# Performance work log

Hardware: AMD Instinct MI355X
Metric: run time of the kernel (lower is better)

The kernel has to match this reference:

```python
import jax, jax.numpy as jnp
import numpy as np

N, E, F, H, EF, ED, L, NL, NH, OD = 2048, 65536, 128, 512, 16, 64, 5, 4, 8, 64
MAX_DEG = 64


def _ln(x, s, b):
    m = x.mean(-1, keepdims=True)
    v = x.var(-1, keepdims=True)
    return (x - m) * jax.lax.rsqrt(v + 1e-5) * s + b


def setup_inputs() -> dict:
    key = jax.random.key(0)
    ks = jax.random.split(key, 40)
    s = 0.02
    x = jax.random.normal(ks[0], (N, F), jnp.float32)
    edge_index = jax.random.randint(ks[1], (2, E), 0, N, jnp.int32)
    edge_attr = jax.random.normal(ks[2], (E, EF), jnp.float32)
    # variable-length shortest paths, padded with -1
    plen = jax.random.randint(ks[3], (N, N), 0, L + 1, jnp.int32)
    pos = jnp.arange(L, dtype=jnp.int32)
    valid = pos[None, None, :] < plen[:, :, None]
    node_paths = jnp.where(valid, jax.random.randint(ks[4], (N, N, L), 0, N, jnp.int32), -1)
    edge_paths = jnp.where(valid, jax.random.randint(ks[5], (N, N, L), 0, E, jnp.int32), -1)
    p = {
        'x': x, 'edge_index': edge_index, 'edge_attr': edge_attr,
        'node_paths': node_paths, 'edge_paths': edge_paths,
        'W_node': s * jax.random.normal(ks[6], (F, H)), 'b_node': jnp.zeros((H,)),
        'W_edge': s * jax.random.normal(ks[7], (EF, ED)), 'b_edge': jnp.zeros((ED,)),
        'z_in': s * jax.random.normal(ks[8], (MAX_DEG, H)),
        'z_out': s * jax.random.normal(ks[9], (MAX_DEG, H)),
        'b_spatial': s * jax.random.normal(ks[10], (L,)),
        'edge_vector': s * jax.random.normal(ks[11], (L, ED)),
        'ln1_s': jnp.ones((NL, H)), 'ln1_b': jnp.zeros((NL, H)),
        'Wq': s * jax.random.normal(ks[12], (NL, H, H)), 'bq': jnp.zeros((NL, H)),
        'Wk': s * jax.random.normal(ks[13], (NL, H, H)), 'bk': jnp.zeros((NL, H)),
        'Wv': s * jax.random.normal(ks[14], (NL, H, H)), 'bv': jnp.zeros((NL, H)),
        'Wo': s * jax.random.normal(ks[15], (NL, H, H)), 'bo': jnp.zeros((NL, H)),
        'ln2_s': jnp.ones((NL, H)), 'ln2_b': jnp.zeros((NL, H)),
        'W1': s * jax.random.normal(ks[16], (NL, H, H)), 'b1': jnp.zeros((NL, H)),
        'W2': s * jax.random.normal(ks[17], (NL, H, H)), 'b2': jnp.zeros((NL, H)),
        'W_out': s * jax.random.normal(ks[18], (H, OD)), 'b_out': jnp.zeros((OD,)),
    }
    return p


def reference(x, edge_index, edge_attr, node_paths, edge_paths,
              W_node, b_node, W_edge, b_edge, z_in, z_out, b_spatial, edge_vector,
              ln1_s, ln1_b, Wq, bq, Wk, bk, Wv, bv, Wo, bo,
              ln2_s, ln2_b, W1, b1, W2, b2, W_out, b_out):
    n = x.shape[0]
    dk = H // NH
    h = x @ W_node + b_node  # [N,H]
    # centrality encoding: in/out degree -> learned embeddings, clamped
    in_deg = jnp.clip(jnp.zeros((n,), jnp.int32).at[edge_index[1]].add(1), 0, MAX_DEG - 1)
    out_deg = jnp.clip(jnp.zeros((n,), jnp.int32).at[edge_index[0]].add(1), 0, MAX_DEG - 1)
    h = h + z_in[in_deg] + z_out[out_deg]
    # edge encoding: mean over path of <edge_vector[k], edge_emb[path_k]>
    e_emb = edge_attr @ W_edge + b_edge           # [E,ED]
    w = e_emb @ edge_vector.T                     # [E,L] per-position dot products
    valid_e = edge_paths >= 0
    gath = w[jnp.clip(edge_paths, 0), jnp.arange(L)[None, None, :]]  # [N,N,L]
    cnt = valid_e.sum(-1).astype(h.dtype)
    c = jnp.where(cnt > 0, (gath * valid_e).sum(-1) / jnp.maximum(cnt, 1.0), 0.0)  # [N,N]
    # spatial encoding: learned scalar per path length
    plen = (node_paths >= 0).sum(-1)
    b_sp = jnp.where(plen > 0, b_spatial[jnp.clip(plen - 1, 0, L - 1)], 0.0)  # [N,N]
    bias = b_sp + c
    scale = 1.0 / jnp.sqrt(jnp.asarray(dk, h.dtype))
    for l in range(NL):
        y = _ln(h, ln1_s[l], ln1_b[l])
        q = (y @ Wq[l] + bq[l]).reshape(n, NH, dk)
        k = (y @ Wk[l] + bk[l]).reshape(n, NH, dk)
        v = (y @ Wv[l] + bv[l]).reshape(n, NH, dk)
        scores = jnp.einsum('ihd,jhd->hij', q, k) * scale + bias[None]
        attn = jax.nn.softmax(scores, axis=-1)
        o = jnp.einsum('hij,jhd->ihd', attn, v).reshape(n, H)
        h = h + o @ Wo[l] + bo[l]
        y2 = _ln(h, ln2_s[l], ln2_b[l])
        h = h + jax.nn.gelu(y2 @ W1[l] + b1[l]) @ W2[l] + b2[l]
    return h @ W_out + b_out
```

## Files before the change

### kernel.cpp

```cpp
#include <hip/hip_runtime.h>
#include <hip/hip_bf16.h>
#include <math.h>

#define N_NODES 2048
#define NEDGE   65536
#define FDIM    128
#define HDIM    512
#define EFD     16
#define EDD     64
#define LPATH   5
#define NLAYER  4
#define NHEAD   8
#define DK      64
#define ODIM    64
#define MAXDEG  64
#define PHALF   2097152

typedef __bf16 bf16;
typedef bf16 bf16x8 __attribute__((ext_vector_type(8)));
typedef bf16 bf16x4 __attribute__((ext_vector_type(4)));
typedef float f32x4 __attribute__((ext_vector_type(4)));
typedef unsigned short u16;
typedef u16 u16x4 __attribute__((ext_vector_type(4)));


__global__ void k_edge_mat(const float* __restrict__ W_edge, const float* __restrict__ b_edge,
                           const float* __restrict__ ev, float* __restrict__ M, float* __restrict__ c5) {
    int t = threadIdx.x;
    if (t < EFD * LPATH) {
        int i = t / LPATH, j = t % LPATH;
        float acc = 0.f;
        for (int k = 0; k < EDD; ++k) acc += W_edge[i * EDD + k] * ev[j * EDD + k];
        M[t] = acc;
    } else if (t >= 80 && t < 80 + LPATH) {
        int j = t - 80;
        float acc = 0.f;
        for (int k = 0; k < EDD; ++k) acc += b_edge[k] * ev[j * EDD + k];
        c5[j] = acc;
    }
}

__global__ __launch_bounds__(256) void k_edge_w(const float* __restrict__ ea, const float* __restrict__ M,
                                                const float* __restrict__ c5, bf16* __restrict__ wT) {
    __shared__ float sM[80];
    __shared__ float sc[8];
    int t = threadIdx.x;
    if (t < 80) sM[t] = M[t];
    if (t < LPATH) sc[t] = c5[t];
    __syncthreads();
    int e = blockIdx.x * 256 + t;
    const float4* p = (const float4*)(ea + (size_t)e * EFD);
    float4 a0 = p[0], a1 = p[1], a2 = p[2], a3 = p[3];
    float a[16] = {a0.x, a0.y, a0.z, a0.w, a1.x, a1.y, a1.z, a1.w,
                   a2.x, a2.y, a2.z, a2.w, a3.x, a3.y, a3.z, a3.w};
    float out[LPATH];
#pragma unroll
    for (int j = 0; j < LPATH; ++j) out[j] = sc[j];
#pragma unroll
    for (int i = 0; i < 16; ++i)
#pragma unroll
        for (int j = 0; j < LPATH; ++j) out[j] += a[i] * sM[i * LPATH + j];
#pragma unroll
    for (int j = 0; j < LPATH; ++j) wT[(size_t)j * NEDGE + e] = (bf16)out[j];
}

__global__ __launch_bounds__(256) void k_deg(const int* __restrict__ ei, int* __restrict__ din, int* __restrict__ dout) {
    int e = blockIdx.x * 256 + threadIdx.x;
    if (e < NEDGE) {
        atomicAdd(&dout[ei[e]], 1);
        atomicAdd(&din[ei[NEDGE + e]], 1);
    }
}

__global__ __launch_bounds__(256) void k_pack(const int* __restrict__ ep, u16* __restrict__ idxp,
                                              unsigned char* __restrict__ maskp) {
    int tid4 = blockIdx.x * 256 + threadIdx.x;
    const int4* p = (const int4*)(ep + (size_t)tid4 * 20);
    int4 q0 = p[0], q1 = p[1], q2 = p[2], q3 = p[3], q4 = p[4];
    int e[20] = {q0.x, q0.y, q0.z, q0.w, q1.x, q1.y, q1.z, q1.w,
                 q2.x, q2.y, q2.z, q2.w, q3.x, q3.y, q3.z, q3.w,
                 q4.x, q4.y, q4.z, q4.w};
    u16x4 out[LPATH];
    unsigned m[4] = {0, 0, 0, 0};
#pragma unroll
    for (int pp = 0; pp < 4; ++pp) {
#pragma unroll
        for (int l = 0; l < LPATH; ++l) {
            int v = e[pp * 5 + l];
            if (v >= 0) m[pp] |= (1u << l);
            out[l][pp] = (u16)v;
        }
    }
#pragma unroll
    for (int l = 0; l < LPATH; ++l)
        *(u16x4*)(idxp + (size_t)l * PHALF + tid4 * 4) = out[l];
    unsigned packed = m[0] | (m[1] << 8) | (m[2] << 16) | (m[3] << 24);
    *(unsigned*)(maskp + (size_t)tid4 * 4) = packed;
}

__global__ __launch_bounds__(1024) void k_bias2(const u16* __restrict__ idxp, const unsigned char* __restrict__ maskp,
                                                const bf16* __restrict__ wT, const float* __restrict__ bsp,
                                                bf16* __restrict__ bias) {
    __shared__ bf16 wsl[NEDGE];
    int t = threadIdx.x;
    int base = blockIdx.x * 8192;
    unsigned char msk[8];
    float csum[8] = {};
#pragma unroll
    for (int r = 0; r < 8; ++r) msk[r] = maskp[base + r * 1024 + t];
    for (int l = 0; l < LPATH; ++l) {
        __syncthreads();
#pragma unroll
        for (int u = 0; u < 4; ++u) {
            int o = u * 16384 + t * 16;
            *(bf16x8*)&wsl[o]     = *(const bf16x8*)&wT[(size_t)l * NEDGE + o];
            *(bf16x8*)&wsl[o + 8] = *(const bf16x8*)&wT[(size_t)l * NEDGE + o + 8];
        }
        u16 ei[8];
#pragma unroll
        for (int r = 0; r < 8; ++r) ei[r] = idxp[(size_t)l * PHALF + base + r * 1024 + t];
        __syncthreads();
#pragma unroll
        for (int r = 0; r < 8; ++r) {
            float v = (float)wsl[ei[r]];
            csum[r] += ((msk[r] >> l) & 1) ? v : 0.f;
        }
    }
#pragma unroll
    for (int r = 0; r < 8; ++r) {
        int cnt = __popc((int)msk[r]);
        float b = cnt ? bsp[cnt - 1] + csum[r] / (float)cnt : 0.f;
        bias[base + r * 1024 + t] = (bf16)b;
    }
}

__global__ __launch_bounds__(256) void k_ln(const float* __restrict__ h, const float* __restrict__ sc,
                                            const float* __restrict__ bi, bf16* __restrict__ y) {
    int i = blockIdx.x, t = threadIdx.x;
    float v0 = h[(size_t)i * HDIM + t];
    float v1 = h[(size_t)i * HDIM + 256 + t];
    float s = v0 + v1, q = v0 * v0 + v1 * v1;
#pragma unroll
    for (int m = 1; m < 64; m <<= 1) { s += __shfl_xor(s, m); q += __shfl_xor(q, m); }
    __shared__ float ssum[4], sq[4];
    int wv = t >> 6;
    if ((t & 63) == 0) { ssum[wv] = s; sq[wv] = q; }
    __syncthreads();
    float S = ssum[0] + ssum[1] + ssum[2] + ssum[3];
    float Q = sq[0] + sq[1] + sq[2] + sq[3];
    float mean = S * (1.f / HDIM);
    float var = Q * (1.f / HDIM) - mean * mean;
    float r = rsqrtf(var + 1e-5f);
    y[(size_t)i * HDIM + t] = (bf16)((v0 - mean) * r * sc[t] + bi[t]);
    y[(size_t)i * HDIM + 256 + t] = (bf16)((v1 - mean) * r * sc[256 + t] + bi[256 + t]);
}

__global__ __launch_bounds__(256) void k_wprep(const float* __restrict__ Wq, const float* __restrict__ Wk,
                                               const float* __restrict__ Wv, const float* __restrict__ Wo,
                                               const float* __restrict__ W1, const float* __restrict__ W2,
                                               bf16* __restrict__ Wt) {
    __shared__ float Ls[64][68];
    int m = blockIdx.y;
    int lay = m / 6, type = m % 6;
    const float* src = type == 0 ? Wq : type == 1 ? Wk : type == 2 ? Wv : type == 3 ? Wo : type == 4 ? W1 : W2;
    src += (size_t)lay * (HDIM * HDIM);
    int q = blockIdx.x;
    int tk = q >> 3, tn = q & 7;
    int t = threadIdx.x;
    int rr = t >> 4, cc = t & 15;
#pragma unroll
    for (int u = 0; u < 4; ++u) {
        float4 v = *(const float4*)(src + (size_t)(tk * 64 + rr + 16 * u) * HDIM + tn * 64 + cc * 4);
        *(float4*)&Ls[rr + 16 * u][cc * 4] = v;
    }
    __syncthreads();
    int nl = t >> 2, kc = t & 3;
    bf16 tmp[16];
#pragma unroll
    for (int u = 0; u < 16; ++u) tmp[u] = (bf16)Ls[kc * 16 + u][nl];
    bf16* dst = Wt + (size_t)m * (HDIM * HDIM) + (size_t)(tn * 64 + nl) * HDIM + tk * 64 + kc * 16;
    *(bf16x8*)(dst) = *(bf16x8*)&tmp[0];
    *(bf16x8*)(dst + 8) = *(bf16x8*)&tmp[8];
}

__global__ __launch_bounds__(256) void k_wprepn(const float* __restrict__ Wn, bf16* __restrict__ WnT) {
    __shared__ float Ls[64][68];
    int b = blockIdx.x;
    int tk = b >> 3, tn = b & 7;
    int t = threadIdx.x, rr = t >> 4, cc = t & 15;
#pragma unroll
    for (int u = 0; u < 4; ++u) {
        float4 v = *(const float4*)(Wn + (size_t)(tk * 64 + rr + 16 * u) * HDIM + tn * 64 + cc * 4);
        *(float4*)&Ls[rr + 16 * u][cc * 4] = v;
    }
    __syncthreads();
    int nl = t >> 2, kc = t & 3;
    bf16 tmp[16];
#pragma unroll
    for (int u = 0; u < 16; ++u) tmp[u] = (bf16)Ls[kc * 16 + u][nl];
    bf16* dst = WnT + (size_t)(tn * 64 + nl) * FDIM + tk * 64 + kc * 16;
    *(bf16x8*)dst = *(bf16x8*)&tmp[0];
    *(bf16x8*)(dst + 8) = *(bf16x8*)&tmp[8];
}

__global__ __launch_bounds__(256) void k_xcast(const float* __restrict__ x, bf16* __restrict__ xb) {
    int i = blockIdx.x * 256 + threadIdx.x;
    float4 v = *(const float4*)(x + (size_t)i * 4);
    bf16x4 o;
    o[0] = (bf16)v.x; o[1] = (bf16)v.y; o[2] = (bf16)v.z; o[3] = (bf16)v.w;
    *(bf16x4*)(xb + (size_t)i * 4) = o;
}

__global__ __launch_bounds__(256) void k_nmm(const bf16* __restrict__ A, const bf16* __restrict__ Bt,
                                             const float* __restrict__ bn, const float* __restrict__ zin,
                                             const float* __restrict__ zout, const int* __restrict__ din,
                                             const int* __restrict__ dout, float* __restrict__ h) {
    __shared__ bf16 Bs[8192];
    int t = threadIdx.x, w = t >> 6, l = t & 63, lr = l & 15, lg = l >> 4;
    int j0 = blockIdx.x * 64, i0 = blockIdx.y * 64;
    const bf16* Bp = Bt + (size_t)j0 * FDIM;
#pragma unroll
    for (int rnd = 0; rnd < 4; ++rnd) {
        int tt = rnd * 256 + t;
        int ks = tt >> 8, qq = (tt >> 6) & 3, mm = (tt >> 2) & 15, gg = tt & 3;
        *(bf16x8*)(Bs + tt * 8) = *(const bf16x8*)(Bp + (size_t)(qq * 16 + mm) * FDIM + ks * 32 + gg * 8);
    }
    __syncthreads();
    const bf16* ap = A + (size_t)(i0 + w * 16 + lr) * FDIM + 8 * lg;
    f32x4 acc[4] = {};
#pragma unroll
    for (int ks = 0; ks < 4; ++ks) {
        bf16x8 a = *(const bf16x8*)(ap + ks * 32);
        const bf16* bb = Bs + ks * 2048 + lr * 32 + lg * 8;
#pragma unroll
        for (int sub = 0; sub < 4; ++sub)
            acc[sub] = __builtin_amdgcn_mfma_f32_16x16x32_bf16(a, *(const bf16x8*)(bb + sub * 512), acc[sub], 0, 0, 0);
    }
#pragma unroll
    for (int r = 0; r < 4; ++r) {
        int i = i0 + w * 16 + lg * 4 + r;
        int di = min(din[i], MAXDEG - 1), dz = min(dout[i], MAXDEG - 1);
#pragma unroll
        for (int sub = 0; sub < 4; ++sub) {
            int j = j0 + sub * 16 + lr;
            h[(size_t)i * HDIM + j] = acc[sub][r] + bn[j] + zin[(size_t)di * HDIM + j] + zout[(size_t)dz * HDIM + j];
        }
    }
}

__global__ __launch_bounds__(256) void k_qkv(const bf16* __restrict__ A, const bf16* __restrict__ Wt_l,
                                             const float* __restrict__ bq, const float* __restrict__ bk,
                                             const float* __restrict__ bv, bf16* __restrict__ qf,
                                             bf16* __restrict__ kf, bf16* __restrict__ vf) {
    __shared__ bf16 Bs[16384];
    int t = threadIdx.x, w = t >> 6, l = t & 63, lr = l & 15, lg = l >> 4;
    int j0 = blockIdx.x * 32, i0 = blockIdx.y * 64;
    int type = j0 >> 9, n0 = j0 & 511;
    const bf16* Bp = Wt_l + (size_t)type * (HDIM * HDIM) + (size_t)n0 * HDIM;
#pragma unroll
    for (int rnd = 0; rnd < 8; ++rnd) {
        int tt = rnd * 256 + t;
        int ks = tt >> 7, qq = (tt >> 6) & 1, mm = (tt >> 2) & 15, gg = tt & 3;
        bf16x8 v = *(const bf16x8*)(Bp + (size_t)(qq * 16 + mm) * HDIM + ks * 32 + gg * 8);
        *(bf16x8*)(Bs + tt * 8) = v;
    }
    __syncthreads();
    const bf16* ap = A + (size_t)(i0 + w * 16 + lr) * HDIM + 8 * lg;
    const float* bvec = (type == 0 ? bq : type == 1 ? bk : bv);
    f32x4 acc[2] = {};
#pragma unroll 4
    for (int ks = 0; ks < 16; ++ks) {
        bf16x8 a  = *(const bf16x8*)(ap + ks * 32);
        const bf16* bb = Bs + ks * 1024 + lr * 32 + lg * 8;
        bf16x8 b0 = *(const bf16x8*)(bb);
        bf16x8 b1 = *(const bf16x8*)(bb + 512);
        acc[0] = __builtin_amdgcn_mfma_f32_16x16x32_bf16(a, b0, acc[0], 0, 0, 0);
        acc[1] = __builtin_amdgcn_mfma_f32_16x16x32_bf16(a, b1, acc[1], 0, 0, 0);
    }
    int h = n0 >> 6;
    if (type < 2) {
        bf16* dst = (type == 0 ? qf : kf);
        int hf = (n0 & 32) >> 5;
        float sc = (type == 0 ? 0.125f : 1.0f);
#pragma unroll
        for (int sub = 0; sub < 2; ++sub) {
#pragma unroll
            for (int r = 0; r < 4; ++r) {
                int i = i0 + w * 16 + lg * 4 + r;
                float v = (acc[sub][r] + bvec[n0 + sub * 16 + lr]) * sc;
                int lgp = sub * 2 + (lr >> 3);
                size_t off = (((size_t)(h * 128 + (i >> 4)) * 2 + hf) << 9) + lgp * 128 + (lg * 4 + r) * 8 + (lr & 7);
                dst[off] = (bf16)v;
            }
        }
    } else {
#pragma unroll
        for (int sub = 0; sub < 2; ++sub) {
#pragma unroll
            for (int r = 0; r < 4; ++r) {
                int node = i0 + w * 16 + lg * 4 + r;
                int dd = (n0 & 63) + sub * 16 + lr;
                float v = acc[sub][r] + bvec[n0 + sub * 16 + lr];
                size_t off = (((size_t)(h * 4 + (dd >> 4)) * 64 + (node >> 5)) << 9)
                           + ((node >> 3) & 3) * 128 + (dd & 15) * 8 + (node & 7);
                vf[off] = (bf16)v;
            }
        }
    }
}

#define FL_RES   1
#define FL_GELU  2
#define FL_OUTF  4

__device__ inline float gelu_f(float x) {
    float x3 = x * x * x;
    float u = 0.7978845608028654f * (x + 0.044715f * x3);
    return 0.5f * x * (1.f + tanhf(u));
}

__global__ __launch_bounds__(1024) void k_mm(const bf16* __restrict__ A, const bf16* __restrict__ Bt,
                                             const float* __restrict__ bvec, const float* __restrict__ res,
                                             float* __restrict__ outF, bf16* __restrict__ outB, int flags) {
    __shared__ bf16 Bs[32768];
    __shared__ float Osh[4][16][68];
    int t = threadIdx.x, w = t >> 6, l = t & 63, lr = l & 15, lg = l >> 4;
    int ti = w & 3, s = w >> 2;
    int j0 = blockIdx.x * 64, i0 = blockIdx.y * 64;
    const bf16* Bp = Bt + (size_t)j0 * HDIM;
#pragma unroll
    for (int rnd = 0; rnd < 4; ++rnd) {
        int tt = rnd * 1024 + t;
        int ks = tt >> 8, qq = (tt >> 6) & 3, mm = (tt >> 2) & 15, gg = tt & 3;
        bf16x8 v = *(const bf16x8*)(Bp + (size_t)(qq * 16 + mm) * HDIM + ks * 32 + gg * 8);
        *(bf16x8*)(Bs + tt * 8) = v;
    }
    __syncthreads();
    const bf16* ap = A + (size_t)(i0 + ti * 16 + lr) * HDIM + 8 * lg;
    f32x4 acc[4] = {};
#pragma unroll
    for (int kk = 0; kk < 4; ++kk) {
        int ks = s * 4 + kk;
        bf16x8 a = *(const bf16x8*)(ap + ks * 32);
        const bf16* bb = Bs + ks * 2048 + lr * 32 + lg * 8;
#pragma unroll
        for (int sub = 0; sub < 4; ++sub) {
            bf16x8 b = *(const bf16x8*)(bb + sub * 512);
            acc[sub] = __builtin_amdgcn_mfma_f32_16x16x32_bf16(a, b, acc[sub], 0, 0, 0);
        }
    }
    if (s == 0) {
#pragma unroll
        for (int sub = 0; sub < 4; ++sub)
#pragma unroll
            for (int r = 0; r < 4; ++r) Osh[ti][lg * 4 + r][sub * 16 + lr] = acc[sub][r];
    }
    __syncthreads();
    if (s == 1) {
#pragma unroll
        for (int sub = 0; sub < 4; ++sub)
#pragma unroll
            for (int r = 0; r < 4; ++r) Osh[ti][lg * 4 + r][sub * 16 + lr] += acc[sub][r];
    }
    __syncthreads();
    if (s == 2) {
#pragma unroll
        for (int sub = 0; sub < 4; ++sub)
#pragma unroll
            for (int r = 0; r < 4; ++r) Osh[ti][lg * 4 + r][sub * 16 + lr] += acc[sub][r];
    }
    __syncthreads();
    if (s == 3) {
#pragma unroll
        for (int sub = 0; sub < 4; ++sub) {
#pragma unroll
            for (int r = 0; r < 4; ++r) {
                int i = i0 + ti * 16 + lg * 4 + r;
                int j = j0 + sub * 16 + lr;
                float v = Osh[ti][lg * 4 + r][sub * 16 + lr] + acc[sub][r] + bvec[j];
                if (flags & FL_RES) v += res[(size_t)i * HDIM + j];
                if (flags & FL_GELU) v = gelu_f(v);
                if (flags & FL_OUTF) outF[(size_t)i * HDIM + j] = v;
                else outB[(size_t)i * HDIM + j] = (bf16)v;
            }
        }
    }
}

__global__ __launch_bounds__(1024) void k_attn2(const bf16* __restrict__ qf, const bf16* __restrict__ kf,
                                                const bf16* __restrict__ vf, const bf16* __restrict__ biasb,
                                                bf16* __restrict__ ob) {
    __shared__ char Pb[16 * 1024];
    __shared__ float Osh[4][64][17];
    __shared__ float Msh[4][4][16], Lsh[4][4][16];
    int t = threadIdx.x, w = t >> 6, l = t & 63, lr = l & 15, lg = l >> 4;
    int ti = w & 3, s = w >> 2;
    int bid = blockIdx.x;
    int wid = (bid & 7) * 32 + (bid >> 3);
    int i0 = (wid >> 3) * 64, hh = wid & 7;
    int irow = i0 + ti * 16;

    const bf16* qb = qf + (((size_t)(hh * 128 + (irow >> 4)) * 2) << 9) + l * 8;
    bf16x8 qy0 = *(const bf16x8*)(qb);
    bf16x8 qy1 = *(const bf16x8*)(qb + 512);

    char* pwr = Pb + w * 1024 + lr * 64;
    unsigned kx = (unsigned)(lr & 6) << 3;

    float m_run = -3e38f, l_run = 0.f;
    f32x4 oacc[4] = {};

    for (int it = 0; it < 16; ++it) {
        int jb = s * 512 + it * 32;
        const bf16* kb = kf + (((size_t)(hh * 128 + (jb >> 4)) * 2) << 9) + l * 8;
        bf16x8 kx00 = *(const bf16x8*)(kb);
        bf16x8 kx01 = *(const bf16x8*)(kb + 512);
        bf16x8 kx10 = *(const bf16x8*)(kb + 1024);
        bf16x8 kx11 = *(const bf16x8*)(kb + 1536);
        const bf16* vb = vf + (((size_t)(hh * 4) * 64 + (jb >> 5)) << 9) + l * 8;
        bf16x8 vx0 = *(const bf16x8*)(vb);
        bf16x8 vx1 = *(const bf16x8*)(vb + 32768);
        bf16x8 vx2 = *(const bf16x8*)(vb + 65536);
        bf16x8 vx3 = *(const bf16x8*)(vb + 98304);
        const bf16* bp = biasb + (size_t)(irow + lr) * N_NODES + jb + lg * 4;
        bf16x4 bv0 = *(const bf16x4*)(bp);
        bf16x4 bv1 = *(const bf16x4*)(bp + 16);

        f32x4 s0v = {}, s1v = {};
        __builtin_amdgcn_s_setprio(1);
        s0v = __builtin_amdgcn_mfma_f32_16x16x32_bf16(kx00, qy0, s0v, 0, 0, 0);
        s0v = __builtin_amdgcn_mfma_f32_16x16x32_bf16(kx01, qy1, s0v, 0, 0, 0);
        s1v = __builtin_amdgcn_mfma_f32_16x16x32_bf16(kx10, qy0, s1v, 0, 0, 0);
        s1v = __builtin_amdgcn_mfma_f32_16x16x32_bf16(kx11, qy1, s1v, 0, 0, 0);
        __builtin_amdgcn_s_setprio(0);

        float p0[4], p1[4];
        float mt = -3e38f;
#pragma unroll
        for (int r = 0; r < 4; ++r) {
            p0[r] = s0v[r] + (float)bv0[r];
            p1[r] = s1v[r] + (float)bv1[r];
            mt = fmaxf(mt, fmaxf(p0[r], p1[r]));
        }
        mt = fmaxf(mt, __shfl_xor(mt, 16));
        mt = fmaxf(mt, __shfl_xor(mt, 32));
        if (!__all(mt <= m_run + 8.f)) {
            float mn = fmaxf(m_run, mt);
            float alpha = __expf(m_run - mn);
            l_run *= alpha;
#pragma unroll
            for (int d = 0; d < 4; ++d) oacc[d] *= alpha;
            m_run = mn;
        }
        float ps = 0.f;
        bf16x4 pk0, pk1;
#pragma unroll
        for (int r = 0; r < 4; ++r) {
            p0[r] = __expf(p0[r] - m_run);
            p1[r] = __expf(p1[r] - m_run);
            ps += p0[r] + p1[r];
            pk0[r] = (bf16)p0[r];
            pk1[r] = (bf16)p1[r];
        }
        ps += __shfl_xor(ps, 16);
        ps += __shfl_xor(ps, 32);
        l_run += ps;

        *(bf16x4*)(pwr + ((lg * 8) ^ kx)) = pk0;
        *(bf16x4*)(pwr + ((32 + lg * 8) ^ kx)) = pk1;
        asm volatile("s_waitcnt lgkmcnt(0)" ::: "memory");
        __builtin_amdgcn_sched_barrier(0x20);
        bf16x8 py = *(bf16x8*)(Pb + w * 1024 + lr * 64 + ((lg * 16) ^ kx));
        __builtin_amdgcn_s_setprio(1);
        oacc[0] = __builtin_amdgcn_mfma_f32_16x16x32_bf16(vx0, py, oacc[0], 0, 0, 0);
        oacc[1] = __builtin_amdgcn_mfma_f32_16x16x32_bf16(vx1, py, oacc[1], 0, 0, 0);
        oacc[2] = __builtin_amdgcn_mfma_f32_16x16x32_bf16(vx2, py, oacc[2], 0, 0, 0);
        oacc[3] = __builtin_amdgcn_mfma_f32_16x16x32_bf16(vx3, py, oacc[3], 0, 0, 0);
        __builtin_amdgcn_s_setprio(0);
    }

    __syncthreads();
    if (lg == 0) { Msh[ti][s][lr] = m_run; Lsh[ti][s][lr] = l_run; }
    __syncthreads();
    float m0 = Msh[ti][0][lr], m1 = Msh[ti][1][lr], m2 = Msh[ti][2][lr], m3 = Msh[ti][3][lr];
    float mtot = fmaxf(fmaxf(m0, m1), fmaxf(m2, m3));
    float l_tot = Lsh[ti][0][lr] * __expf(m0 - mtot) + Lsh[ti][1][lr] * __expf(m1 - mtot)
                + Lsh[ti][2][lr] * __expf(m2 - mtot) + Lsh[ti][3][lr] * __expf(m3 - mtot);
    float fac = __expf(m_run - mtot);
#pragma unroll
    for (int d = 0; d < 4; ++d) oacc[d] *= fac;
    if (s == 0) {
#pragma unroll
        for (int db = 0; db < 4; ++db)
#pragma unroll
            for (int r = 0; r < 4; ++r) Osh[ti][db * 16 + lg * 4 + r][lr] = oacc[db][r];
    }
    __syncthreads();
    if (s == 1) {
#pragma unroll
        for (int db = 0; db < 4; ++db)
#pragma unroll
            for (int r = 0; r < 4; ++r) Osh[ti][db * 16 + lg * 4 + r][lr] += oacc[db][r];
    }
    __syncthreads();
    if (s == 2) {
#pragma unroll
        for (int db = 0; db < 4; ++db)
#pragma unroll
            for (int r = 0; r < 4; ++r) Osh[ti][db * 16 + lg * 4 + r][lr] += oacc[db][r];
    }
    __syncthreads();
    if (s == 3) {
        float inv = 1.f / l_tot;
#pragma unroll
        for (int db = 0; db < 4; ++db) {
            bf16x4 o4;
#pragma unroll
            for (int r = 0; r < 4; ++r)
                o4[r] = (bf16)((Osh[ti][db * 16 + lg * 4 + r][lr] + oacc[db][r]) * inv);
            *(bf16x4*)(ob + (size_t)(irow + lr) * HDIM + hh * DK + db * 16 + lg * 4) = o4;
        }
    }
}

__global__ __launch_bounds__(256) void k_gemm(const float* __restrict__ A, const float* __restrict__ B,
                                              const float* __restrict__ bvec, float* __restrict__ C,
                                              int M, int Nc, int K) {
    __shared__ float As[16][68];
    __shared__ float Bs[16][68];
    int t = threadIdx.x;
    int tm = t >> 4, tn = t & 15;
    int i0 = blockIdx.y * 64, j0 = blockIdx.x * 64;
    int ar = t >> 2, aq = t & 3;
    int br = t >> 4, bq = t & 15;
    float acc[4][4] = {};
    for (int k0 = 0; k0 < K; k0 += 16) {
        float4 av = *(const float4*)(A + (size_t)(i0 + ar) * K + k0 + aq * 4);
        As[aq * 4 + 0][ar] = av.x;
        As[aq * 4 + 1][ar] = av.y;
        As[aq * 4 + 2][ar] = av.z;
        As[aq * 4 + 3][ar] = av.w;
        *(float4*)&Bs[br][bq * 4] = *(const float4*)(B + (size_t)(k0 + br) * Nc + j0 + bq * 4);
        __syncthreads();
#pragma unroll
        for (int k = 0; k < 16; ++k) {
            float4 a4 = *(const float4*)&As[k][tm * 4];
            float4 b4 = *(const float4*)&Bs[k][tn * 4];
            float avv[4] = {a4.x, a4.y, a4.z, a4.w};
            float bvv[4] = {b4.x, b4.y, b4.z, b4.w};
#pragma unroll
            for (int r = 0; r < 4; ++r)
#pragma unroll
                for (int c = 0; c < 4; ++c) acc[r][c] += avv[r] * bvv[c];
        }
        __syncthreads();
    }
#pragma unroll
    for (int r = 0; r < 4; ++r) {
#pragma unroll
        for (int c = 0; c < 4; ++c) {
            int i = i0 + tm * 4 + r;
            int j = j0 + tn * 4 + c;
            C[(size_t)i * Nc + j] = acc[r][c] + bvec[j];
        }
    }
}

extern "C" void kernel_launch(void* const* d_in, const int* in_sizes, int n_in,
                              void* d_out, int out_size, void* d_ws, size_t ws_size,
                              hipStream_t stream) {
    const float* x      = (const float*)d_in[0];
    const int*   ei     = (const int*)d_in[1];
    const float* eattr  = (const float*)d_in[2];
    const int*   epaths = (const int*)d_in[4];
    const float* Wn     = (const float*)d_in[5];
    const float* bn     = (const float*)d_in[6];
    const float* We     = (const float*)d_in[7];
    const float* be     = (const float*)d_in[8];
    const float* zin    = (const float*)d_in[9];
    const float* zout   = (const float*)d_in[10];
    const float* bsp    = (const float*)d_in[11];
    const float* ev     = (const float*)d_in[12];
    const float* ln1s   = (const float*)d_in[13];
    const float* ln1b   = (const float*)d_in[14];
    const float* Wq     = (const float*)d_in[15];
    const float* bq     = (const float*)d_in[16];
    const float* Wk     = (const float*)d_in[17];
    const float* bk     = (const float*)d_in[18];
    const float* Wv     = (const float*)d_in[19];
    const float* bv     = (const float*)d_in[20];
    const float* Wo     = (const float*)d_in[21];
    const float* bo     = (const float*)d_in[22];
    const float* ln2s   = (const float*)d_in[23];
    const float* ln2b   = (const float*)d_in[24];
    const float* W1     = (const float*)d_in[25];
    const float* b1     = (const float*)d_in[26];
    const float* W2     = (const float*)d_in[27];
    const float* b2     = (const float*)d_in[28];
    const float* Wout   = (const float*)d_in[29];
    const float* bout   = (const float*)d_in[30];

    char* base = (char*)d_ws;
    size_t off = 0;
    auto alloc = [&](size_t bytes) { char* p = base + off; off = (off + bytes + 255) & ~(size_t)255; return p; };
    bf16*  bias   = (bf16*)alloc((size_t)N_NODES * N_NODES * 2);
    float* h      = (float*)alloc((size_t)N_NODES * HDIM * 4);
    bf16*  wT     = (bf16*)alloc((size_t)LPATH * NEDGE * 2);
    float* Mb     = (float*)alloc(96 * 4);
    float* c5     = (float*)alloc(16 * 4);
    int*   deg    = (int*)alloc(2 * N_NODES * 4);
    bf16*  xbf    = (bf16*)alloc((size_t)N_NODES * FDIM * 2);
    bf16*  WnT    = (bf16*)alloc((size_t)HDIM * FDIM * 2);
    char*  region = alloc(26u * 1024 * 1024);
    u16*   idxp   = (u16*)region;
    unsigned char* maskp = (unsigned char*)(region + (size_t)LPATH * PHALF * 2);
    bf16*  Wt     = (bf16*)region;
    bf16*  y_bf   = Wt + (size_t)NLAYER * 6 * HDIM * HDIM;
    bf16*  qfb    = y_bf + (size_t)N_NODES * HDIM;
    bf16*  kfb    = qfb + (size_t)N_NODES * HDIM / 2 * 2;
    bf16*  vfb    = kfb + (size_t)NHEAD * 128 * 2 * 512;
    bf16*  ob_bf  = vfb + (size_t)NHEAD * 4 * 64 * 512;
    bf16*  t1_bf  = ob_bf + (size_t)N_NODES * HDIM;
    int* din = deg;
    int* dout = deg + N_NODES;

    hipMemsetAsync(deg, 0, 2 * N_NODES * sizeof(int), stream);

    k_edge_mat<<<1, 128, 0, stream>>>(We, be, ev, Mb, c5);
    k_edge_w<<<NEDGE / 256, 256, 0, stream>>>(eattr, Mb, c5, wT);
    k_deg<<<NEDGE / 256, 256, 0, stream>>>(ei, din, dout);

    for (int half = 0; half < 2; ++half) {
        k_pack<<<PHALF / 1024, 256, 0, stream>>>(epaths + (size_t)half * PHALF * 5, idxp, maskp);
        k_bias2<<<256, 1024, 0, stream>>>(idxp, maskp, wT, bsp, bias + (size_t)half * PHALF);
    }

    k_wprep<<<dim3(64, 24), 256, 0, stream>>>(Wq, Wk, Wv, Wo, W1, W2, Wt);
    k_wprepn<<<16, 256, 0, stream>>>(Wn, WnT);
    k_xcast<<<(N_NODES * FDIM) / 1024, 256, 0, stream>>>(x, xbf);
    k_nmm<<<dim3(8, 32), 256, 0, stream>>>(xbf, WnT, bn, zin, zout, din, dout, h);

    dim3 gqkv(48, 32);
    dim3 gmm(8, 32);

    for (int lay = 0; lay < NLAYER; ++lay) {
        const bf16* Wt_l = Wt + (size_t)lay * 6 * HDIM * HDIM;
        size_t bOff = (size_t)lay * HDIM;
        k_ln<<<N_NODES, 256, 0, stream>>>(h, ln1s + bOff, ln1b + bOff, y_bf);
        k_qkv<<<gqkv, 256, 0, stream>>>(y_bf, Wt_l, bq + bOff, bk + bOff, bv + bOff, qfb, kfb, vfb);
        k_attn2<<<256, 1024, 0, stream>>>(qfb, kfb, vfb, bias, ob_bf);
        k_mm<<<gmm, 1024, 0, stream>>>(ob_bf, Wt_l + (size_t)3 * HDIM * HDIM, bo + bOff, h, h, nullptr, FL_RES | FL_OUTF);
        k_ln<<<N_NODES, 256, 0, stream>>>(h, ln2s + bOff, ln2b + bOff, y_bf);
        k_mm<<<gmm, 1024, 0, stream>>>(y_bf, Wt_l + (size_t)4 * HDIM * HDIM, b1 + bOff, nullptr, nullptr, t1_bf, FL_GELU);
        k_mm<<<gmm, 1024, 0, stream>>>(t1_bf, Wt_l + (size_t)5 * HDIM * HDIM, b2 + bOff, h, h, nullptr, FL_RES | FL_OUTF);
    }
    k_gemm<<<dim3(1, 32), 256, 0, stream>>>(h, Wout, bout, (float*)d_out, N_NODES, ODIM, HDIM);
}
```

Before: 501.7 us.

## Fuse LN2 into FFN1 GEMM, merge prep kernels, and unsplit path packing

Several independent changes. The edge matrix precompute is folded into k_edge_w, and the x-to-bf16 cast is folded into the node GEMM. Path packing now runs in one pass over all paths, staging loads through shared memory, instead of two halves. The second layernorm is fused into the first FFN GEMM by computing row statistics inside a new k_mmln kernel. Launch count and intermediate traffic go down, at the cost of separate workspace buffers, which no longer alias each other, and larger shared memory in the fused kernel.

```diff
diff --git a/kernel.cpp b/kernel.cpp
--- a/kernel.cpp
+++ b/kernel.cpp
@@ -14,7 +14,7 @@
 #define DK      64
 #define ODIM    64
 #define MAXDEG  64
-#define PHALF   2097152
+#define PTOT    4194304
 
 typedef __bf16 bf16;
 typedef bf16 bf16x8 __attribute__((ext_vector_type(8)));
@@ -23,30 +23,23 @@
 typedef unsigned short u16;
 typedef u16 u16x4 __attribute__((ext_vector_type(4)));
 
-
-__global__ void k_edge_mat(const float* __restrict__ W_edge, const float* __restrict__ b_edge,
-                           const float* __restrict__ ev, float* __restrict__ M, float* __restrict__ c5) {
-    int t = threadIdx.x;
-    if (t < EFD * LPATH) {
-        int i = t / LPATH, j = t % LPATH;
-        float acc = 0.f;
-        for (int k = 0; k < EDD; ++k) acc += W_edge[i * EDD + k] * ev[j * EDD + k];
-        M[t] = acc;
-    } else if (t >= 80 && t < 80 + LPATH) {
-        int j = t - 80;
-        float acc = 0.f;
-        for (int k = 0; k < EDD; ++k) acc += b_edge[k] * ev[j * EDD + k];
-        c5[j] = acc;
-    }
-}
-
-__global__ __launch_bounds__(256) void k_edge_w(const float* __restrict__ ea, const float* __restrict__ M,
-                                                const float* __restrict__ c5, bf16* __restrict__ wT) {
+__global__ __launch_bounds__(256) void k_edge_w(const float* __restrict__ ea, const float* __restrict__ We,
+                                                const float* __restrict__ be, const float* __restrict__ ev,
+                                                bf16* __restrict__ wT) {
     __shared__ float sM[80];
     __shared__ float sc[8];
     int t = threadIdx.x;
-    if (t < 80) sM[t] = M[t];
-    if (t < LPATH) sc[t] = c5[t];
+    if (t < 80) {
+        int i = t / 5, j = t % 5;
+        float acc = 0.f;
+        for (int k = 0; k < EDD; ++k) acc += We[i * EDD + k] * ev[j * EDD + k];
+        sM[t] = acc;
+    } else if (t >= 128 && t < 128 + LPATH) {
+        int j = t - 128;
+        float acc = 0.f;
+        for (int k = 0; k < EDD; ++k) acc += be[k] * ev[j * EDD + k];
+        sc[j] = acc;
+    }
     __syncthreads();
     int e = blockIdx.x * 256 + t;
     const float4* p = (const float4*)(ea + (size_t)e * EFD);
@@ -74,28 +67,29 @@
 
 __global__ __launch_bounds__(256) void k_pack(const int* __restrict__ ep, u16* __restrict__ idxp,
                                               unsigned char* __restrict__ maskp) {
-    int tid4 = blockIdx.x * 256 + threadIdx.x;
-    const int4* p = (const int4*)(ep + (size_t)tid4 * 20);
-    int4 q0 = p[0], q1 = p[1], q2 = p[2], q3 = p[3], q4 = p[4];
-    int e[20] = {q0.x, q0.y, q0.z, q0.w, q1.x, q1.y, q1.z, q1.w,
-                 q2.x, q2.y, q2.z, q2.w, q3.x, q3.y, q3.z, q3.w,
-                 q4.x, q4.y, q4.z, q4.w};
+    __shared__ int ints[5120];
+    int t = threadIdx.x;
+    size_t blk = blockIdx.x;
+    const int4* src = (const int4*)(ep + blk * 5120);
+#pragma unroll
+    for (int u = 0; u < 5; ++u) *(int4*)&ints[(t + 256 * u) * 4] = src[t + 256 * u];
+    __syncthreads();
     u16x4 out[LPATH];
     unsigned m[4] = {0, 0, 0, 0};
 #pragma unroll
-    for (int pp = 0; pp < 4; ++pp) {
+    for (int j = 0; j < 4; ++j) {
+        int p = t * 4 + j;
 #pragma unroll
         for (int l = 0; l < LPATH; ++l) {
-            int v = e[pp * 5 + l];
-            if (v >= 0) m[pp] |= (1u << l);
-            out[l][pp] = (u16)v;
+            int v = ints[p * 5 + l];
+            if (v >= 0) m[j] |= (1u << l);
+            out[l][j] = (u16)v;
         }
     }
 #pragma unroll
     for (int l = 0; l < LPATH; ++l)
-        *(u16x4*)(idxp + (size_t)l * PHALF + tid4 * 4) = out[l];
-    unsigned packed = m[0] | (m[1] << 8) | (m[2] << 16) | (m[3] << 24);
-    *(unsigned*)(maskp + (size_t)tid4 * 4) = packed;
+        *(u16x4*)(idxp + (size_t)l * PTOT + blk * 1024 + t * 4) = out[l];
+    *(unsigned*)(maskp + blk * 1024 + t * 4) = m[0] | (m[1] << 8) | (m[2] << 16) | (m[3] << 24);
 }
 
 __global__ __launch_bounds__(1024) void k_bias2(const u16* __restrict__ idxp, const unsigned char* __restrict__ maskp,
@@ -118,7 +112,7 @@
         }
         u16 ei[8];
 #pragma unroll
-        for (int r = 0; r < 8; ++r) ei[r] = idxp[(size_t)l * PHALF + base + r * 1024 + t];
+        for (int r = 0; r < 8; ++r) ei[r] = idxp[(size_t)l * PTOT + base + r * 1024 + t];
         __syncthreads();
 #pragma unroll
         for (int r = 0; r < 8; ++r) {
@@ -203,15 +197,7 @@
     *(bf16x8*)(dst + 8) = *(bf16x8*)&tmp[8];
 }
 
-__global__ __launch_bounds__(256) void k_xcast(const float* __restrict__ x, bf16* __restrict__ xb) {
-    int i = blockIdx.x * 256 + threadIdx.x;
-    float4 v = *(const float4*)(x + (size_t)i * 4);
-    bf16x4 o;
-    o[0] = (bf16)v.x; o[1] = (bf16)v.y; o[2] = (bf16)v.z; o[3] = (bf16)v.w;
-    *(bf16x4*)(xb + (size_t)i * 4) = o;
-}
-
-__global__ __launch_bounds__(256) void k_nmm(const bf16* __restrict__ A, const bf16* __restrict__ Bt,
+__global__ __launch_bounds__(256) void k_nmm(const float* __restrict__ x, const bf16* __restrict__ Bt,
                                              const float* __restrict__ bn, const float* __restrict__ zin,
                                              const float* __restrict__ zout, const int* __restrict__ din,
                                              const int* __restrict__ dout, float* __restrict__ h) {
@@ -226,11 +212,15 @@
         *(bf16x8*)(Bs + tt * 8) = *(const bf16x8*)(Bp + (size_t)(qq * 16 + mm) * FDIM + ks * 32 + gg * 8);
     }
     __syncthreads();
-    const bf16* ap = A + (size_t)(i0 + w * 16 + lr) * FDIM + 8 * lg;
+    const float* ap = x + (size_t)(i0 + w * 16 + lr) * FDIM + 8 * lg;
     f32x4 acc[4] = {};
 #pragma unroll
     for (int ks = 0; ks < 4; ++ks) {
-        bf16x8 a = *(const bf16x8*)(ap + ks * 32);
+        float4 f0 = *(const float4*)(ap + ks * 32);
+        float4 f1 = *(const float4*)(ap + ks * 32 + 4);
+        bf16x8 a;
+        a[0] = (bf16)f0.x; a[1] = (bf16)f0.y; a[2] = (bf16)f0.z; a[3] = (bf16)f0.w;
+        a[4] = (bf16)f1.x; a[5] = (bf16)f1.y; a[6] = (bf16)f1.z; a[7] = (bf16)f1.w;
         const bf16* bb = Bs + ks * 2048 + lr * 32 + lg * 8;
 #pragma unroll
         for (int sub = 0; sub < 4; ++sub)
@@ -382,6 +372,104 @@
                 if (flags & FL_GELU) v = gelu_f(v);
                 if (flags & FL_OUTF) outF[(size_t)i * HDIM + j] = v;
                 else outB[(size_t)i * HDIM + j] = (bf16)v;
+            }
+        }
+    }
+}
+
+__global__ __launch_bounds__(1024) void k_mmln(const float* __restrict__ h, const bf16* __restrict__ Bt,
+                                               const float* __restrict__ lnS, const float* __restrict__ lnB,
+                                               const float* __restrict__ bvec, bf16* __restrict__ outB) {
+    __shared__ bf16 As[32768];
+    __shared__ bf16 Bs[32768];
+    __shared__ float Osh[4][16][68];
+    __shared__ float sbuf[HDIM], bbuf[HDIM];
+    int t = threadIdx.x, w = t >> 6, l = t & 63, lr = l & 15, lg = l >> 4;
+    int ti = w & 3, s = w >> 2;
+    int j0 = blockIdx.x * 64, i0 = blockIdx.y * 64;
+    if (t < HDIM) sbuf[t] = lnS[t];
+    else bbuf[t - HDIM] = lnB[t - HDIM];
+    const bf16* Bp = Bt + (size_t)j0 * HDIM;
+#pragma unroll
+    for (int rnd = 0; rnd < 4; ++rnd) {
+        int tt = rnd * 1024 + t;
+        int ks = tt >> 8, qq = (tt >> 6) & 3, mm = (tt >> 2) & 15, gg = tt & 3;
+        *(bf16x8*)(Bs + tt * 8) = *(const bf16x8*)(Bp + (size_t)(qq * 16 + mm) * HDIM + ks * 32 + gg * 8);
+    }
+    int row = t >> 4, ksc = t & 15;
+    const float* hp = h + (size_t)(i0 + row) * HDIM + ksc * 32;
+    float4 hv[8];
+    float S = 0.f, Q = 0.f;
+#pragma unroll
+    for (int u = 0; u < 8; ++u) {
+        hv[u] = *(const float4*)(hp + u * 4);
+        S += hv[u].x + hv[u].y + hv[u].z + hv[u].w;
+        Q += hv[u].x * hv[u].x + hv[u].y * hv[u].y + hv[u].z * hv[u].z + hv[u].w * hv[u].w;
+    }
+#pragma unroll
+    for (int m = 1; m < 16; m <<= 1) { S += __shfl_xor(S, m); Q += __shfl_xor(Q, m); }
+    float mean = S * (1.f / HDIM);
+    float var = Q * (1.f / HDIM) - mean * mean;
+    float rr = rsqrtf(var + 1e-5f);
+    float ca = rr, cc = -mean * rr;
+    __syncthreads();
+    {
+        bf16 tmp[32];
+#pragma unroll
+        for (int u = 0; u < 8; ++u) {
+            float vv[4] = {hv[u].x, hv[u].y, hv[u].z, hv[u].w};
+#pragma unroll
+            for (int c = 0; c < 4; ++c) {
+                int col = ksc * 32 + u * 4 + c;
+                tmp[u * 4 + c] = (bf16)(fmaf(fmaf(vv[c], ca, cc), sbuf[col], bbuf[col]));
+            }
+        }
+        bf16* dst = As + (row >> 4) * 8192 + ksc * 512 + (row & 15) * 32;
+#pragma unroll
+        for (int u = 0; u < 4; ++u) *(bf16x8*)(dst + u * 8) = *(bf16x8*)&tmp[u * 8];
+    }
+    __syncthreads();
+    const bf16* apl = As + ti * 8192 + lr * 32 + lg * 8;
+    f32x4 acc[4] = {};
+#pragma unroll
+    for (int kk = 0; kk < 4; ++kk) {
+        int ks = s * 4 + kk;
+        bf16x8 a = *(const bf16x8*)(apl + ks * 512);
+        const bf16* bb = Bs + ks * 2048 + lr * 32 + lg * 8;
+#pragma unroll
+        for (int sub = 0; sub < 4; ++sub)
+            acc[sub] = __builtin_amdgcn_mfma_f32_16x16x32_bf16(a, *(const bf16x8*)(bb + sub * 512), acc[sub], 0, 0, 0);
+    }
+    if (s == 0) {
+#pragma unroll
+        for (int sub = 0; sub < 4; ++sub)
+#pragma unroll
+            for (int r = 0; r < 4; ++r) Osh[ti][lg * 4 + r][sub * 16 + lr] = acc[sub][r];
+    }
+    __syncthreads();
+    if (s == 1) {
+#pragma unroll
+        for (int sub = 0; sub < 4; ++sub)
+#pragma unroll
+            for (int r = 0; r < 4; ++r) Osh[ti][lg * 4 + r][sub * 16 + lr] += acc[sub][r];
+    }
+    __syncthreads();
+    if (s == 2) {
+#pragma unroll
+        for (int sub = 0; sub < 4; ++sub)
+#pragma unroll
+            for (int r = 0; r < 4; ++r) Osh[ti][lg * 4 + r][sub * 16 + lr] += acc[sub][r];
+    }
+    __syncthreads();
+    if (s == 3) {
+#pragma unroll
+        for (int sub = 0; sub < 4; ++sub) {
+#pragma unroll
+            for (int r = 0; r < 4; ++r) {
+                int i = i0 + ti * 16 + lg * 4 + r;
+                int j = j0 + sub * 16 + lr;
+                float v = gelu_f(Osh[ti][lg * 4 + r][sub * 16 + lr] + acc[sub][r] + bvec[j]);
+                outB[(size_t)i * HDIM + j] = (bf16)v;
             }
         }
     }
@@ -606,39 +694,29 @@
     bf16*  bias   = (bf16*)alloc((size_t)N_NODES * N_NODES * 2);
     float* h      = (float*)alloc((size_t)N_NODES * HDIM * 4);
     bf16*  wT     = (bf16*)alloc((size_t)LPATH * NEDGE * 2);
-    float* Mb     = (float*)alloc(96 * 4);
-    float* c5     = (float*)alloc(16 * 4);
     int*   deg    = (int*)alloc(2 * N_NODES * 4);
-    bf16*  xbf    = (bf16*)alloc((size_t)N_NODES * FDIM * 2);
+    u16*   idxp   = (u16*)alloc((size_t)LPATH * PTOT * 2);
+    unsigned char* maskp = (unsigned char*)alloc((size_t)PTOT);
     bf16*  WnT    = (bf16*)alloc((size_t)HDIM * FDIM * 2);
-    char*  region = alloc(26u * 1024 * 1024);
-    u16*   idxp   = (u16*)region;
-    unsigned char* maskp = (unsigned char*)(region + (size_t)LPATH * PHALF * 2);
-    bf16*  Wt     = (bf16*)region;
-    bf16*  y_bf   = Wt + (size_t)NLAYER * 6 * HDIM * HDIM;
-    bf16*  qfb    = y_bf + (size_t)N_NODES * HDIM;
-    bf16*  kfb    = qfb + (size_t)N_NODES * HDIM / 2 * 2;
-    bf16*  vfb    = kfb + (size_t)NHEAD * 128 * 2 * 512;
-    bf16*  ob_bf  = vfb + (size_t)NHEAD * 4 * 64 * 512;
-    bf16*  t1_bf  = ob_bf + (size_t)N_NODES * HDIM;
+    bf16*  Wt     = (bf16*)alloc((size_t)NLAYER * 6 * HDIM * HDIM * 2);
+    bf16*  y_bf   = (bf16*)alloc((size_t)N_NODES * HDIM * 2);
+    bf16*  qfb    = (bf16*)alloc((size_t)NHEAD * 128 * 2 * 512 * 2);
+    bf16*  kfb    = (bf16*)alloc((size_t)NHEAD * 128 * 2 * 512 * 2);
+    bf16*  vfb    = (bf16*)alloc((size_t)NHEAD * 4 * 64 * 512 * 2);
+    bf16*  ob_bf  = (bf16*)alloc((size_t)N_NODES * HDIM * 2);
+    bf16*  t1_bf  = (bf16*)alloc((size_t)N_NODES * HDIM * 2);
     int* din = deg;
     int* dout = deg + N_NODES;
 
     hipMemsetAsync(deg, 0, 2 * N_NODES * sizeof(int), stream);
 
-    k_edge_mat<<<1, 128, 0, stream>>>(We, be, ev, Mb, c5);
-    k_edge_w<<<NEDGE / 256, 256, 0, stream>>>(eattr, Mb, c5, wT);
+    k_edge_w<<<NEDGE / 256, 256, 0, stream>>>(eattr, We, be, ev, wT);
     k_deg<<<NEDGE / 256, 256, 0, stream>>>(ei, din, dout);
-
-    for (int half = 0; half < 2; ++half) {
-        k_pack<<<PHALF / 1024, 256, 0, stream>>>(epaths + (size_t)half * PHALF * 5, idxp, maskp);
-        k_bias2<<<256, 1024, 0, stream>>>(idxp, maskp, wT, bsp, bias + (size_t)half * PHALF);
-    }
-
+    k_pack<<<PTOT / 1024, 256, 0, stream>>>(epaths, idxp, maskp);
+    k_bias2<<<512, 1024, 0, stream>>>(idxp, maskp, wT, bsp, bias);
     k_wprep<<<dim3(64, 24), 256, 0, stream>>>(Wq, Wk, Wv, Wo, W1, W2, Wt);
     k_wprepn<<<16, 256, 0, stream>>>(Wn, WnT);
-    k_xcast<<<(N_NODES * FDIM) / 1024, 256, 0, stream>>>(x, xbf);
-    k_nmm<<<dim3(8, 32), 256, 0, stream>>>(xbf, WnT, bn, zin, zout, din, dout, h);
+    k_nmm<<<dim3(8, 32), 256, 0, stream>>>(x, WnT, bn, zin, zout, din, dout, h);
 
     dim3 gqkv(48, 32);
     dim3 gmm(8, 32);
@@ -650,8 +728,7 @@
         k_qkv<<<gqkv, 256, 0, stream>>>(y_bf, Wt_l, bq + bOff, bk + bOff, bv + bOff, qfb, kfb, vfb);
         k_attn2<<<256, 1024, 0, stream>>>(qfb, kfb, vfb, bias, ob_bf);
         k_mm<<<gmm, 1024, 0, stream>>>(ob_bf, Wt_l + (size_t)3 * HDIM * HDIM, bo + bOff, h, h, nullptr, FL_RES | FL_OUTF);
-        k_ln<<<N_NODES, 256, 0, stream>>>(h, ln2s + bOff, ln2b + bOff, y_bf);
-        k_mm<<<gmm, 1024, 0, stream>>>(y_bf, Wt_l + (size_t)4 * HDIM * HDIM, b1 + bOff, nullptr, nullptr, t1_bf, FL_GELU);
+        k_mmln<<<gmm, 1024, 0, stream>>>(h, Wt_l + (size_t)4 * HDIM * HDIM, ln2s + bOff, ln2b + bOff, b1 + bOff, t1_bf);
         k_mm<<<gmm, 1024, 0, stream>>>(t1_bf, Wt_l + (size_t)5 * HDIM * HDIM, b2 + bOff, h, h, nullptr, FL_RES | FL_OUTF);
     }
     k_gemm<<<dim3(1, 32), 256, 0, stream>>>(h, Wout, bout, (float*)d_out, N_NODES, ODIM, HDIM);
```

Result: no change. 506.5 us (+1.0%).
